# Performance work log

Hardware: AMD Instinct MI355X
Metric: run time of the kernel (lower is better)

The kernel has to match this reference:

```python
import jax, jax.numpy as jnp
import numpy as np

W = 5      # window size
H = 4      # num heads (num_channels)
EPS = 1e-6

def rmsnorm(x, w):
    return x * w * jax.lax.rsqrt(jnp.mean(x * x, axis=-1, keepdims=True) + EPS)

def dwconv3d(x, k):
    # x: [B,D0,D1,D2,C], k: [3,3,3,1,C] depthwise 3x3x3 conv, SAME padding
    return jax.lax.conv_general_dilated(
        x, k, (1, 1, 1), 'SAME',
        dimension_numbers=('NDHWC', 'DHWIO', 'NDHWC'),
        feature_group_count=x.shape[-1])

def _part(t):
    # [B,D0,D1,D2,C] -> [B*nw, W^3, C] non-overlapping 3D windows
    B, D0, D1, D2, C = t.shape
    t = t.reshape(B, D0 // W, W, D1 // W, W, D2 // W, W, C)
    t = t.transpose(0, 1, 3, 5, 2, 4, 6, 7)
    return t.reshape(-1, W ** 3, C)

def _unpart(t, B, D0, D1, D2):
    C = t.shape[-1]
    t = t.reshape(B, D0 // W, D1 // W, D2 // W, W, W, W, C)
    t = t.transpose(0, 1, 4, 2, 5, 3, 6, 7)
    return t.reshape(B, D0, D1, D2, C)

def _pool01(t):
    # mean-pool poolable_dims=(0,1) by factor W -> coarse grid
    B, D0, D1, D2, C = t.shape
    return t.reshape(B, D0 // W, W, D1 // W, W, D2, C).mean(axis=(2, 4))

def _mha(q, k, v):
    # q,k,v: [N, L, C] -> [N, L, C] multi-head attention
    N, L, C = q.shape
    dh = C // H
    q = q.reshape(N, L, H, dh)
    k = k.reshape(N, L, H, dh)
    v = v.reshape(N, L, H, dh)
    s = jnp.einsum('nqhd,nkhd->nhqk', q, k) * (1.0 / np.sqrt(dh))
    p = jax.nn.softmax(s, axis=-1)
    return jnp.einsum('nhqk,nkhd->nqhd', p, v).reshape(N, L, C)

def _hier_attn(x, qkv_w, qkv_b, proj_w, proj_b, dw_pre, dw_post, lr_down, lr_up):
    B, D0, D1, D2, C = x.shape
    # conv_position='both': pre depthwise-conv positional term
    xin = x + dwconv3d(x, dw_pre)
    qkv = xin @ qkv_w + qkv_b                     # [B,D0,D1,D2,3C]
    q, k, v = jnp.split(qkv, 3, axis=-1)
    # fine scale: windowed local attention in W^3 blocks
    fine = _unpart(_mha(_part(q), _part(k), _part(v)), B, D0, D1, D2)
    # coarse scale: pool dims (0,1) by W, global attention over coarse tokens
    qc, kc, vc = _pool01(q), _pool01(k), _pool01(v)
    Nc = qc.shape[1] * qc.shape[2] * qc.shape[3]
    oc = _mha(qc.reshape(B, Nc, C), kc.reshape(B, Nc, C), vc.reshape(B, Nc, C))
    oc = oc.reshape(B, D0 // W, D1 // W, D2, C)
    oc = jnp.repeat(jnp.repeat(oc, W, axis=1), W, axis=2)   # upsample to full grid
    # lowrank hierarchical merge of coarse branch into fine branch
    merged = fine + (oc @ lr_down) @ lr_up
    out = merged @ proj_w + proj_b
    out = out + xin                               # attn_residual
    out = out + dwconv3d(out, dw_post)            # post conv position
    return out

def setup_inputs() -> dict:
    key = jax.random.key(0)
    ks = jax.random.split(key, 8)
    B, D0, D1, D2, C = 4, 40, 40, 20, 256
    rank = C // 4
    s = 0.02
    return {
        'x': jax.random.normal(ks[0], (B, D0, D1, D2, C), jnp.float32),
        'norm1_w': jnp.ones((C,), jnp.float32),
        'attn_norm_w': jnp.ones((C,), jnp.float32),
        'qkv_w': jax.random.normal(ks[1], (C, 3 * C), jnp.float32) * s,
        'qkv_b': jnp.zeros((3 * C,), jnp.float32),
        'proj_w': jax.random.normal(ks[2], (C, C), jnp.float32) * s,
        'proj_b': jnp.zeros((C,), jnp.float32),
        'dw_pre': jax.random.normal(ks[3], (3, 3, 3, 1, C), jnp.float32) * s,
        'dw_post': jax.random.normal(ks[4], (3, 3, 3, 1, C), jnp.float32) * s,
        'lr_down': jax.random.normal(ks[5], (C, rank), jnp.float32) * s,
        'lr_up': jax.random.normal(ks[6], (rank, C), jnp.float32) * s,
    }

def reference(x, norm1_w, attn_norm_w, qkv_w, qkv_b, proj_w, proj_b,
              dw_pre, dw_post, lr_down, lr_up) -> jnp.ndarray:
    # x = x + attn_norm(hier_attn(norm1(x)))   (dropout inactive in eval)
    a = _hier_attn(rmsnorm(x, norm1_w), qkv_w, qkv_b, proj_w, proj_b,
                   dw_pre, dw_post, lr_down, lr_up)
    return x + rmsnorm(a, attn_norm_w)
```

## Files before the change

### kernel.cpp

```cpp
#include <hip/hip_runtime.h>

#define D0c 40
#define D1c 40
#define D2c 20
#define NVOX 128000

typedef __attribute__((ext_vector_type(4))) float f4;
typedef __attribute__((ext_vector_type(8))) __bf16 bf8;
typedef __attribute__((ext_vector_type(8))) unsigned short u8s;

static __device__ __forceinline__ unsigned short f2bf(float f) {
  union { float f; unsigned int u; } v; v.f = f;
  unsigned int r = v.u + 0x7fffu + ((v.u >> 16) & 1u);
  return (unsigned short)(r >> 16);
}
static __device__ __forceinline__ float bf2f(unsigned short h) {
  union { unsigned int u; float f; } v; v.u = ((unsigned int)h) << 16;
  return v.f;
}

#define MFMA16(a, b, c) __builtin_amdgcn_mfma_f32_16x16x32_bf16((a), (b), (c), 0, 0, 0)

static __device__ __forceinline__ void gload16(const void* g, void* l) {
  __builtin_amdgcn_global_load_lds((const __attribute__((address_space(1))) unsigned int*)g,
                                   (__attribute__((address_space(3))) unsigned int*)l, 16, 0, 0);
}

__global__ __launch_bounds__(256) void k_prepw(const float* __restrict__ qkv_w,
                                               const float* __restrict__ proj_w,
                                               unsigned short* __restrict__ wq,
                                               unsigned short* __restrict__ wp) {
  int id = blockIdx.x * 256 + threadIdx.x;
  if (id < 768 * 256) {
    int kk = id & 31, row = (id >> 5) & 127, kc = (id >> 12) & 7, nt = id >> 15;
    int s = kk >> 3, kj = kk & 7;
    int g = s ^ ((row >> 1) & 3);
    int k = kc * 32 + g * 8 + kj;
    int n = nt * 128 + row;
    wq[id] = f2bf(qkv_w[k * 768 + n]);
  } else {
    int j = id - 768 * 256;
    int kk = j & 31, row = (j >> 5) & 127, kc = (j >> 12) & 7, nt = j >> 15;
    int s = kk >> 3, kj = kk & 7;
    int g = s ^ ((row >> 1) & 3);
    int k = kc * 32 + g * 8 + kj;
    int n = nt * 128 + row;
    wp[j] = f2bf(proj_w[k * 256 + n]);
  }
}

__global__ __launch_bounds__(256) void k_rms1(const float* __restrict__ x,
                                              const float* __restrict__ w,
                                              unsigned short* __restrict__ xn) {
  int wv = threadIdx.x >> 6, ln = threadIdx.x & 63;
  int n = blockIdx.x * 4 + wv;
  f4 v = ((const f4*)(x + (size_t)n * 256))[ln];
  float ss = v.x * v.x + v.y * v.y + v.z * v.z + v.w * v.w;
#pragma unroll
  for (int m = 32; m >= 1; m >>= 1) ss += __shfl_xor(ss, m);
  float rs = rsqrtf(ss * (1.f / 256.f) + 1e-6f);
  f4 wv4 = ((const f4*)w)[ln];
  ushort4 o;
  o.x = f2bf(v.x * wv4.x * rs); o.y = f2bf(v.y * wv4.y * rs);
  o.z = f2bf(v.z * wv4.z * rs); o.w = f2bf(v.w * wv4.w * rs);
  ((ushort4*)(xn + (size_t)n * 256))[ln] = o;
}

__global__ __launch_bounds__(256) void k_convpre(const unsigned short* __restrict__ xn,
                                                 const float* __restrict__ dw,
                                                 unsigned short* __restrict__ xin) {
  __shared__ float wl[6912];
  for (int i = threadIdx.x; i < 6912; i += 256) wl[i] = dw[i];
  __syncthreads();
  int wv = threadIdx.x >> 6, ln = threadIdx.x & 63;
  int col = blockIdx.x * 4 + wv;
  int z1 = col % D1c; int t = col / D1c; int z0 = t % D0c; int b = t / D0c;
  int c0 = ln * 4;

  const unsigned short* base[9];
  bool val[9];
#pragma unroll
  for (int c = 0; c < 9; c++) {
    int dy = c / 3 - 1, dx = c % 3 - 1;
    int y0 = z0 + dy, y1 = z1 + dx;
    val[c] = ((unsigned)y0 < (unsigned)D0c) && ((unsigned)y1 < (unsigned)D1c);
    int yy0 = val[c] ? y0 : z0, yy1 = val[c] ? y1 : z1;
    base[c] = xn + ((size_t)((b * D0c + yy0) * D1c + yy1) * D2c) * 256 + c0;
  }
  f4 a0 = {0.f,0.f,0.f,0.f}, a1 = {0.f,0.f,0.f,0.f}, a2 = {0.f,0.f,0.f,0.f};
  ushort4 nxt[9];
#pragma unroll
  for (int c = 0; c < 9; c++) {
    ushort4 ld = {0, 0, 0, 0};
    if (val[c]) ld = *(const ushort4*)(base[c]);
    nxt[c] = ld;
  }
  unsigned short* op = xin + ((size_t)col * D2c) * 256 + c0;

  for (int z = 0; z < 20; z++) {
    f4 cf[9];
#pragma unroll
    for (int c = 0; c < 9; c++) {
      cf[c].x = bf2f(nxt[c].x); cf[c].y = bf2f(nxt[c].y);
      cf[c].z = bf2f(nxt[c].z); cf[c].w = bf2f(nxt[c].w);
    }
    int zn = (z < 19) ? (z + 1) : 19;
#pragma unroll
    for (int c = 0; c < 9; c++) {
      ushort4 ld = {0, 0, 0, 0};
      if (val[c]) ld = *(const ushort4*)(base[c] + (size_t)zn * 256);
      nxt[c] = ld;
    }
#pragma unroll
    for (int c = 0; c < 9; c++) {
      const f4 w0 = *(const f4*)&wl[(c * 3 + 0) * 256 + c0];
      const f4 w1 = *(const f4*)&wl[(c * 3 + 1) * 256 + c0];
      const f4 w2 = *(const f4*)&wl[(c * 3 + 2) * 256 + c0];
      a0.x += w2.x * cf[c].x; a0.y += w2.y * cf[c].y; a0.z += w2.z * cf[c].z; a0.w += w2.w * cf[c].w;
      a1.x += w1.x * cf[c].x; a1.y += w1.y * cf[c].y; a1.z += w1.z * cf[c].z; a1.w += w1.w * cf[c].w;
      a2.x += w0.x * cf[c].x; a2.y += w0.y * cf[c].y; a2.z += w0.z * cf[c].z; a2.w += w0.w * cf[c].w;
    }
    a1.x += cf[4].x; a1.y += cf[4].y; a1.z += cf[4].z; a1.w += cf[4].w;
    if (z >= 1) {
      ushort4 o;
      o.x = f2bf(a0.x); o.y = f2bf(a0.y); o.z = f2bf(a0.z); o.w = f2bf(a0.w);
      *(ushort4*)op = o;
      op += 256;
    }
    a0 = a1; a1 = a2; a2 = (f4){0.f,0.f,0.f,0.f};
  }
  {
    ushort4 o;
    o.x = f2bf(a0.x); o.y = f2bf(a0.y); o.z = f2bf(a0.z); o.w = f2bf(a0.w);
    *(ushort4*)op = o;
  }
}

__global__ __launch_bounds__(256) void k_gemm_qkv(const unsigned short* __restrict__ a_bf,
                                                  const unsigned short* __restrict__ wq2,
                                                  const float* __restrict__ bias,
                                                  unsigned short* __restrict__ out) {
  __shared__ unsigned short As[16384];
  __shared__ unsigned short Bs[8192];
  int m0 = blockIdx.x * 64;
  int tid = threadIdx.x;
  int w = tid >> 6, l = tid & 63;
  int wr = w >> 1, wc = w & 1;
  int lrow = l & 15, lg = l >> 4;

  {
    const char* Ab = (const char*)(a_bf + (size_t)m0 * 256);
    int row = tid >> 2, s = tid & 3;
    int g = s ^ ((row >> 1) & 3);
    const char* src0 = Ab + row * 512 + g * 16;
    char* dst0 = ((char*)As) + w * 1024 + l * 16;
#pragma unroll
    for (int kc = 0; kc < 8; kc++)
      gload16(src0 + kc * 64, dst0 + kc * 4096);
  }
  {
    const char* gB = (const char*)wq2;
    char* lB = (char*)Bs;
    gload16(gB + tid * 16, lB + w * 1024 + l * 16);
    gload16(gB + 4096 + tid * 16, lB + 4096 + w * 1024 + l * 16);
  }

  int buf = 0;
  f4 acc[2][4];
  for (int nt = 0; nt < 6; nt++) {
    float bvv[4];
#pragma unroll
    for (int j = 0; j < 4; j++) bvv[j] = bias[nt * 128 + wc * 64 + j * 16 + lrow];
#pragma unroll
    for (int i = 0; i < 2; i++)
#pragma unroll
      for (int j = 0; j < 4; j++) acc[i][j] = {0.f, 0.f, 0.f, 0.f};

    for (int kc = 0; kc < 8; kc++) {
      int t = nt * 8 + kc;
      if (t + 1 < 48) {
        const char* gB = (const char*)wq2 + (size_t)(t + 1) * 8192;
        char* lB = ((char*)Bs) + (buf ^ 1) * 8192;
        gload16(gB + tid * 16, lB + w * 1024 + l * 16);
        gload16(gB + 4096 + tid * 16, lB + 4096 + w * 1024 + l * 16);
        asm volatile("s_waitcnt vmcnt(2)\n\ts_barrier" ::: "memory");
      } else {
        asm volatile("s_waitcnt vmcnt(0)\n\ts_barrier" ::: "memory");
      }
      bf8 af[2], bf_[4];
#pragma unroll
      for (int i = 0; i < 2; i++) {
        int row = wr * 32 + i * 16 + lrow;
        af[i] = *(const bf8*)&As[kc * 2048 + row * 32 + ((lg ^ ((row >> 1) & 3)) * 8)];
      }
#pragma unroll
      for (int j = 0; j < 4; j++) {
        int rowb = wc * 64 + j * 16 + lrow;
        bf_[j] = *(const bf8*)&Bs[buf * 4096 + rowb * 32 + ((lg ^ ((rowb >> 1) & 3)) * 8)];
      }
#pragma unroll
      for (int i = 0; i < 2; i++)
#pragma unroll
        for (int j = 0; j < 4; j++) acc[i][j] = MFMA16(af[i], bf_[j], acc[i][j]);
      asm volatile("s_barrier" ::: "memory");
      buf ^= 1;
    }

    unsigned short* Cs = &Bs[(buf ^ 1) * 4096];
    int crow = tid >> 3, cseg = tid & 7;
#pragma unroll
    for (int h = 0; h < 2; h++) {
      if (wr == h) {
#pragma unroll
        for (int i = 0; i < 2; i++)
#pragma unroll
          for (int j = 0; j < 4; j++)
#pragma unroll
            for (int r = 0; r < 4; r++)
              Cs[(i * 16 + lg * 4 + r) * 128 + wc * 64 + j * 16 + lrow] =
                  f2bf(acc[i][j][r] + bvv[j]);
      }
      asm volatile("s_waitcnt lgkmcnt(0)\n\ts_barrier" ::: "memory");
      {
        u8s v0 = *(const u8s*)&Cs[crow * 128 + cseg * 16];
        u8s v1 = *(const u8s*)&Cs[crow * 128 + cseg * 16 + 8];
        unsigned short* orow = out + (size_t)(m0 + h * 32 + crow) * 768 + nt * 128 + cseg * 16;
        *(u8s*)orow = v0;
        *(u8s*)(orow + 8) = v1;
      }
      asm volatile("s_waitcnt lgkmcnt(0)\n\ts_barrier" ::: "memory");
    }
  }
}

__global__ __launch_bounds__(256) void k_fineattn(const unsigned short* __restrict__ qkv,
                                                  unsigned short* __restrict__ fine) {
  __shared__ unsigned short sm[27136];
  unsigned short* Qs = sm;
  unsigned short* Ks = sm + 9216;
  unsigned short* Vt = sm + 18432;
  unsigned short* Ps = sm;
  int h = blockIdx.x & 3, wid = blockIdx.x >> 2;
  int w2 = wid & 3, w1 = (wid >> 2) & 7, w0 = (wid >> 5) & 7, b = wid >> 8;
  int tid = threadIdx.x;
  int tok = tid >> 1, half = tid & 1;
  if (tok < 125) {
    int i0 = tok / 25, rr = tok % 25, i1 = rr / 5, i2 = rr % 5;
    int n = ((b * D0c + w0 * 5 + i0) * D1c + w1 * 5 + i1) * D2c + w2 * 5 + i2;
    const u8s* qp = (const u8s*)(qkv + (size_t)n * 768 + h * 64 + half * 32);
    const u8s* kp = (const u8s*)(qkv + (size_t)n * 768 + 256 + h * 64 + half * 32);
    const unsigned short* vp = qkv + (size_t)n * 768 + 512 + h * 64 + half * 32;
#pragma unroll
    for (int e = 0; e < 4; e++) {
      *(u8s*)&Qs[tok * 72 + half * 32 + e * 8] = qp[e];
      *(u8s*)&Ks[tok * 72 + half * 32 + e * 8] = kp[e];
    }
#pragma unroll
    for (int d = 0; d < 32; d++) Vt[(half * 32 + d) * 136 + tok] = vp[d];
  } else {
    u8s z = {0, 0, 0, 0, 0, 0, 0, 0};
#pragma unroll
    for (int e = 0; e < 4; e++) {
      *(u8s*)&Qs[tok * 72 + half * 32 + e * 8] = z;
      *(u8s*)&Ks[tok * 72 + half * 32 + e * 8] = z;
    }
#pragma unroll
    for (int d = 0; d < 32; d++) Vt[(half * 32 + d) * 136 + tok] = 0;
  }
  __syncthreads();
  int wv = tid >> 6, ln = tid & 63, lrow = ln & 15, lg = ln >> 4;
  f4 s[2][8];
#pragma unroll
  for (int mi = 0; mi < 2; mi++)
#pragma unroll
    for (int ni = 0; ni < 8; ni++) s[mi][ni] = {0.f, 0.f, 0.f, 0.f};
  bf8 aq[2][2];
#pragma unroll
  for (int ks = 0; ks < 2; ks++)
#pragma unroll
    for (int mi = 0; mi < 2; mi++)
      aq[mi][ks] = *(const bf8*)&Qs[(wv * 32 + mi * 16 + lrow) * 72 + ks * 32 + lg * 8];
#pragma unroll
  for (int ni = 0; ni < 8; ni++) {
#pragma unroll
    for (int ks = 0; ks < 2; ks++) {
      bf8 bk = *(const bf8*)&Ks[(ni * 16 + lrow) * 72 + ks * 32 + lg * 8];
      s[0][ni] = MFMA16(aq[0][ks], bk, s[0][ni]);
      s[1][ni] = MFMA16(aq[1][ks], bk, s[1][ni]);
    }
  }
#pragma unroll
  for (int mi = 0; mi < 2; mi++) {
#pragma unroll
    for (int j = 0; j < 4; j++) {
      float mx = -3e38f;
#pragma unroll
      for (int ni = 0; ni < 8; ni++) {
        int col = ni * 16 + lrow;
        float v = (col < 125) ? s[mi][ni][j] * 0.125f : -3e38f;
        s[mi][ni][j] = v;
        mx = fmaxf(mx, v);
      }
#pragma unroll
      for (int m = 8; m >= 1; m >>= 1) mx = fmaxf(mx, __shfl_xor(mx, m));
      float sum = 0.f;
#pragma unroll
      for (int ni = 0; ni < 8; ni++) {
        float p = __expf(s[mi][ni][j] - mx);
        s[mi][ni][j] = p;
        sum += p;
      }
#pragma unroll
      for (int m = 8; m >= 1; m >>= 1) sum += __shfl_xor(sum, m);
      float inv = 1.f / sum;
#pragma unroll
      for (int ni = 0; ni < 8; ni++) s[mi][ni][j] *= inv;
    }
  }
  __syncthreads();
#pragma unroll
  for (int mi = 0; mi < 2; mi++)
#pragma unroll
    for (int ni = 0; ni < 8; ni++)
#pragma unroll
      for (int j = 0; j < 4; j++)
        Ps[(wv * 32 + mi * 16 + lg * 4 + j) * 136 + ni * 16 + lrow] = f2bf(s[mi][ni][j]);
  __syncthreads();
  f4 o[2][4];
#pragma unroll
  for (int mi = 0; mi < 2; mi++)
#pragma unroll
    for (int ni = 0; ni < 4; ni++) o[mi][ni] = {0.f, 0.f, 0.f, 0.f};
#pragma unroll
  for (int ks = 0; ks < 4; ks++) {
    bf8 ap0 = *(const bf8*)&Ps[(wv * 32 + 0 + lrow) * 136 + ks * 32 + lg * 8];
    bf8 ap1 = *(const bf8*)&Ps[(wv * 32 + 16 + lrow) * 136 + ks * 32 + lg * 8];
#pragma unroll
    for (int ni = 0; ni < 4; ni++) {
      bf8 bv = *(const bf8*)&Vt[(ni * 16 + lrow) * 136 + ks * 32 + lg * 8];
      o[0][ni] = MFMA16(ap0, bv, o[0][ni]);
      o[1][ni] = MFMA16(ap1, bv, o[1][ni]);
    }
  }
#pragma unroll
  for (int mi = 0; mi < 2; mi++) {
    int rt0 = wv * 32 + mi * 16 + lg * 4;
#pragma unroll
    for (int r = 0; r < 4; r++) {
      int tk = rt0 + r;
      if (tk >= 125) continue;
      int i0 = tk / 25, rr = tk % 25, i1 = rr / 5, i2 = rr % 5;
      int n = ((b * D0c + w0 * 5 + i0) * D1c + w1 * 5 + i1) * D2c + w2 * 5 + i2;
#pragma unroll
      for (int ni = 0; ni < 4; ni++)
        fine[(size_t)n * 256 + h * 64 + ni * 16 + lrow] = f2bf(o[mi][ni][r]);
    }
  }
}

__global__ __launch_bounds__(256) void k_pool(const unsigned short* __restrict__ qkv,
                                              unsigned short* __restrict__ qc,
                                              unsigned short* __restrict__ kc,
                                              unsigned short* __restrict__ vct) {
  int ct = blockIdx.x;
  int z2 = ct % 20; int t = ct / 20; int c1 = t & 7; int c0 = (t >> 3) & 7; int b = t >> 6;
  int tid = threadIdx.x;
  float a0 = 0.f, a1 = 0.f, a2 = 0.f;
  for (int i0 = 0; i0 < 5; i0++)
    for (int i1 = 0; i1 < 5; i1++) {
      int n = ((b * D0c + c0 * 5 + i0) * D1c + c1 * 5 + i1) * D2c + z2;
      const unsigned short* row = qkv + (size_t)n * 768;
      a0 += bf2f(row[tid]);
      a1 += bf2f(row[tid + 256]);
      a2 += bf2f(row[tid + 512]);
    }
  const float sc = 1.f / 25.f;
  qc[(size_t)ct * 256 + tid] = f2bf(a0 * sc);
  kc[(size_t)ct * 256 + tid] = f2bf(a1 * sc);
  int h = tid >> 6, d = tid & 63;
  int tk = ct - b * 1280;
  vct[(((size_t)b * 4 + h) * 64 + d) * 1288 + tk] = f2bf(a2 * sc);
}

__global__ __launch_bounds__(256) void k_coarse(const unsigned short* __restrict__ qc,
                                                const unsigned short* __restrict__ kc,
                                                const unsigned short* __restrict__ vct,
                                                float* __restrict__ oc) {
  __shared__ unsigned short Qs[9216];
  __shared__ unsigned short KP[9216];
  __shared__ unsigned short Vts[4608];
  int qt = blockIdx.x;
  int b = blockIdx.y >> 2, h = blockIdx.y & 3;
  int tid = threadIdx.x, wv = tid >> 6, ln = tid & 63, lrow = ln & 15, lg = ln >> 4;
  {
    int tk = tid >> 1, half = tid & 1;
    const u8s* qp = (const u8s*)(qc + (size_t)(b * 1280 + qt * 128 + tk) * 256 + h * 64 + half * 32);
#pragma unroll
    for (int e = 0; e < 4; e++) *(u8s*)&Qs[tk * 72 + half * 32 + e * 8] = qp[e];
  }
  float mrun[2][4], srun[2][4];
  f4 o[2][4];
#pragma unroll
  for (int mi = 0; mi < 2; mi++)
#pragma unroll
    for (int j = 0; j < 4; j++) { mrun[mi][j] = -3e38f; srun[mi][j] = 0.f; }
#pragma unroll
  for (int mi = 0; mi < 2; mi++)
#pragma unroll
    for (int ni = 0; ni < 4; ni++) o[mi][ni] = {0.f, 0.f, 0.f, 0.f};

  int ktok = tid >> 2, kq = (tid & 3) * 16;
  int vd = tid >> 2, vtc = (tid & 3) * 16;

  for (int kt = 0; kt < 20; kt++) {
    {
      const u8s* kp = (const u8s*)(kc + (size_t)(b * 1280 + kt * 64 + ktok) * 256 + h * 64 + kq);
      *(u8s*)&KP[ktok * 72 + kq] = kp[0];
      *(u8s*)&KP[ktok * 72 + kq + 8] = kp[1];
      const u8s* vp = (const u8s*)(vct + (((size_t)b * 4 + h) * 64 + vd) * 1288 + kt * 64 + vtc);
      *(u8s*)&Vts[vd * 72 + vtc] = vp[0];
      *(u8s*)&Vts[vd * 72 + vtc + 8] = vp[1];
    }
    __syncthreads();
    f4 s[2][4];
#pragma unroll
    for (int mi = 0; mi < 2; mi++)
#pragma unroll
      for (int ni = 0; ni < 4; ni++) s[mi][ni] = {0.f, 0.f, 0.f, 0.f};
    bf8 aq[2][2];
#pragma unroll
    for (int ks = 0; ks < 2; ks++)
#pragma unroll
      for (int mi = 0; mi < 2; mi++)
        aq[mi][ks] = *(const bf8*)&Qs[(wv * 32 + mi * 16 + lrow) * 72 + ks * 32 + lg * 8];
#pragma unroll
    for (int ni = 0; ni < 4; ni++) {
#pragma unroll
      for (int ks = 0; ks < 2; ks++) {
        bf8 bk = *(const bf8*)&KP[(ni * 16 + lrow) * 72 + ks * 32 + lg * 8];
        s[0][ni] = MFMA16(aq[0][ks], bk, s[0][ni]);
        s[1][ni] = MFMA16(aq[1][ks], bk, s[1][ni]);
      }
    }
#pragma unroll
    for (int mi = 0; mi < 2; mi++) {
#pragma unroll
      for (int j = 0; j < 4; j++) {
        float mx = -3e38f;
#pragma unroll
        for (int ni = 0; ni < 4; ni++) {
          float v = s[mi][ni][j] * 0.125f;
          s[mi][ni][j] = v;
          mx = fmaxf(mx, v);
        }
#pragma unroll
        for (int m = 8; m >= 1; m >>= 1) mx = fmaxf(mx, __shfl_xor(mx, m));
        float nm = fmaxf(mrun[mi][j], mx);
        float alpha = __expf(mrun[mi][j] - nm);
        mrun[mi][j] = nm;
        float sum = 0.f;
#pragma unroll
        for (int ni = 0; ni < 4; ni++) {
          float p = __expf(s[mi][ni][j] - nm);
          s[mi][ni][j] = p;
          sum += p;
        }
#pragma unroll
        for (int m = 8; m >= 1; m >>= 1) sum += __shfl_xor(sum, m);
        srun[mi][j] = srun[mi][j] * alpha + sum;
#pragma unroll
        for (int ni = 0; ni < 4; ni++) o[mi][ni][j] *= alpha;
      }
    }
    __syncthreads();
#pragma unroll
    for (int mi = 0; mi < 2; mi++)
#pragma unroll
      for (int ni = 0; ni < 4; ni++)
#pragma unroll
        for (int j = 0; j < 4; j++)
          KP[(wv * 32 + mi * 16 + lg * 4 + j) * 72 + ni * 16 + lrow] = f2bf(s[mi][ni][j]);
    __syncthreads();
#pragma unroll
    for (int ks = 0; ks < 2; ks++) {
      bf8 ap0 = *(const bf8*)&KP[(wv * 32 + 0 + lrow) * 72 + ks * 32 + lg * 8];
      bf8 ap1 = *(const bf8*)&KP[(wv * 32 + 16 + lrow) * 72 + ks * 32 + lg * 8];
#pragma unroll
      for (int ni = 0; ni < 4; ni++) {
        bf8 bv = *(const bf8*)&Vts[(ni * 16 + lrow) * 72 + ks * 32 + lg * 8];
        o[0][ni] = MFMA16(ap0, bv, o[0][ni]);
        o[1][ni] = MFMA16(ap1, bv, o[1][ni]);
      }
    }
    __syncthreads();
  }
#pragma unroll
  for (int mi = 0; mi < 2; mi++)
#pragma unroll
    for (int j = 0; j < 4; j++) {
      float inv = 1.f / srun[mi][j];
      int row = qt * 128 + wv * 32 + mi * 16 + lg * 4 + j;
      float* orow = oc + ((size_t)(b * 1280 + row)) * 256 + h * 64;
#pragma unroll
      for (int ni = 0; ni < 4; ni++) orow[ni * 16 + lrow] = o[mi][ni][j] * inv;
    }
}

__global__ __launch_bounds__(256) void k_lowrank(const float* __restrict__ oc,
                                                 const float* __restrict__ lrd,
                                                 const float* __restrict__ lru,
                                                 float* __restrict__ oclr) {
  __shared__ float tmp[16 * 64];
  int t0 = blockIdx.x * 16;
  int tid = threadIdx.x;
  int i = tid >> 4, r4 = (tid & 15) * 4;
  f4 a = {0.f, 0.f, 0.f, 0.f};
  const float* orow = oc + (size_t)(t0 + i) * 256;
  for (int k = 0; k < 256; k++) {
    float ov = orow[k];
    const f4 w = *(const f4*)&lrd[k * 64 + r4];
    a.x += ov * w.x; a.y += ov * w.y; a.z += ov * w.z; a.w += ov * w.w;
  }
  *(f4*)&tmp[i * 64 + r4] = a;
  __syncthreads();
  int c16 = (tid & 15) * 16;
  f4 acc0 = {0.f,0.f,0.f,0.f}, acc1 = {0.f,0.f,0.f,0.f}, acc2 = {0.f,0.f,0.f,0.f}, acc3 = {0.f,0.f,0.f,0.f};
  for (int r = 0; r < 64; r++) {
    float tv = tmp[i * 64 + r];
    const f4* wr = (const f4*)&lru[r * 256 + c16];
    f4 w0 = wr[0], w1 = wr[1], w2 = wr[2], w3 = wr[3];
    acc0.x += tv * w0.x; acc0.y += tv * w0.y; acc0.z += tv * w0.z; acc0.w += tv * w0.w;
    acc1.x += tv * w1.x; acc1.y += tv * w1.y; acc1.z += tv * w1.z; acc1.w += tv * w1.w;
    acc2.x += tv * w2.x; acc2.y += tv * w2.y; acc2.z += tv * w2.z; acc2.w += tv * w2.w;
    acc3.x += tv * w3.x; acc3.y += tv * w3.y; acc3.z += tv * w3.z; acc3.w += tv * w3.w;
  }
  float* outr = oclr + (size_t)(t0 + i) * 256 + c16;
  *(f4*)&outr[0] = acc0; *(f4*)&outr[4] = acc1; *(f4*)&outr[8] = acc2; *(f4*)&outr[12] = acc3;
}

__global__ __launch_bounds__(256) void k_gemm_proj(const unsigned short* __restrict__ fine,
                                                   const float* __restrict__ oclr,
                                                   const unsigned short* __restrict__ wp2,
                                                   const float* __restrict__ bias,
                                                   const unsigned short* __restrict__ xin,
                                                   unsigned short* __restrict__ out1) {
  __shared__ unsigned short As[16384];
  __shared__ unsigned short Bs[8192];
  int m0 = blockIdx.x * 64;
  int tid = threadIdx.x;
  int w = tid >> 6, l = tid & 63;
  int wr = w >> 1, wc = w & 1;
  int lrow = l & 15, lg = l >> 4;

  {
    const char* gB = (const char*)wp2;
    char* lB = (char*)Bs;
    gload16(gB + tid * 16, lB + w * 1024 + l * 16);
    gload16(gB + 4096 + tid * 16, lB + 4096 + w * 1024 + l * 16);
  }
  {
    int row = tid >> 2, s = tid & 3;
    int g = s ^ ((row >> 1) & 3);
    int nrow = m0 + row;
    int z2 = nrow % D2c; int tt = nrow / D2c; int z1 = tt % D1c; tt /= D1c;
    int z0 = tt % D0c; int bb = tt / D0c;
    int ct = ((bb * 8 + z0 / 5) * 8 + z1 / 5) * 20 + z2;
    const unsigned short* fp = fine + (size_t)nrow * 256 + g * 8;
    const float* cp = oclr + (size_t)ct * 256 + g * 8;
#pragma unroll
    for (int kc = 0; kc < 8; kc++) {
      u8s fv = *(const u8s*)(fp + kc * 32);
      f4 cv0 = *(const f4*)(cp + kc * 32);
      f4 cv1 = *(const f4*)(cp + kc * 32 + 4);
      u8s t0;
      t0[0] = f2bf(bf2f(fv[0]) + cv0.x); t0[1] = f2bf(bf2f(fv[1]) + cv0.y);
      t0[2] = f2bf(bf2f(fv[2]) + cv0.z); t0[3] = f2bf(bf2f(fv[3]) + cv0.w);
      t0[4] = f2bf(bf2f(fv[4]) + cv1.x); t0[5] = f2bf(bf2f(fv[5]) + cv1.y);
      t0[6] = f2bf(bf2f(fv[6]) + cv1.z); t0[7] = f2bf(bf2f(fv[7]) + cv1.w);
      *(u8s*)&As[kc * 2048 + row * 32 + s * 8] = t0;
    }
  }
  asm volatile("s_waitcnt lgkmcnt(0)\n\ts_barrier" ::: "memory");

  int buf = 0;
  f4 acc[2][4];
  for (int nt = 0; nt < 2; nt++) {
    float bvv[4];
#pragma unroll
    for (int j = 0; j < 4; j++) bvv[j] = bias[nt * 128 + wc * 64 + j * 16 + lrow];
#pragma unroll
    for (int i = 0; i < 2; i++)
#pragma unroll
      for (int j = 0; j < 4; j++) acc[i][j] = {0.f, 0.f, 0.f, 0.f};

    for (int kc = 0; kc < 8; kc++) {
      int t = nt * 8 + kc;
      if (t + 1 < 16) {
        const char* gB = (const char*)wp2 + (size_t)(t + 1) * 8192;
        char* lB = ((char*)Bs) + (buf ^ 1) * 8192;
        gload16(gB + tid * 16, lB + w * 1024 + l * 16);
        gload16(gB + 4096 + tid * 16, lB + 4096 + w * 1024 + l * 16);
        asm volatile("s_waitcnt vmcnt(2)\n\ts_barrier" ::: "memory");
      } else {
        asm volatile("s_waitcnt vmcnt(0)\n\ts_barrier" ::: "memory");
      }
      bf8 af[2], bf_[4];
#pragma unroll
      for (int i = 0; i < 2; i++) {
        int row = wr * 32 + i * 16 + lrow;
        af[i] = *(const bf8*)&As[kc * 2048 + row * 32 + ((lg ^ ((row >> 1) & 3)) * 8)];
      }
#pragma unroll
      for (int j = 0; j < 4; j++) {
        int rowb = wc * 64 + j * 16 + lrow;
        bf_[j] = *(const bf8*)&Bs[buf * 4096 + rowb * 32 + ((lg ^ ((rowb >> 1) & 3)) * 8)];
      }
#pragma unroll
      for (int i = 0; i < 2; i++)
#pragma unroll
        for (int j = 0; j < 4; j++) acc[i][j] = MFMA16(af[i], bf_[j], acc[i][j]);
      asm volatile("s_barrier" ::: "memory");
      buf ^= 1;
    }

    unsigned short* Cs = &Bs[(buf ^ 1) * 4096];
    int crow = tid >> 3, cseg = tid & 7;
#pragma unroll
    for (int h = 0; h < 2; h++) {
      if (wr == h) {
#pragma unroll
        for (int i = 0; i < 2; i++)
#pragma unroll
          for (int j = 0; j < 4; j++)
#pragma unroll
            for (int r = 0; r < 4; r++)
              Cs[(i * 16 + lg * 4 + r) * 128 + wc * 64 + j * 16 + lrow] =
                  f2bf(acc[i][j][r] + bvv[j]);
      }
      asm volatile("s_waitcnt lgkmcnt(0)\n\ts_barrier" ::: "memory");
      {
        u8s v0 = *(const u8s*)&Cs[crow * 128 + cseg * 16];
        u8s v1 = *(const u8s*)&Cs[crow * 128 + cseg * 16 + 8];
        const unsigned short* xrow = xin + (size_t)(m0 + h * 32 + crow) * 256 + nt * 128 + cseg * 16;
        u8s x0 = *(const u8s*)xrow;
        u8s x1 = *(const u8s*)(xrow + 8);
        u8s o0, o1;
#pragma unroll
        for (int e = 0; e < 8; e++) {
          o0[e] = f2bf(bf2f(v0[e]) + bf2f(x0[e]));
          o1[e] = f2bf(bf2f(v1[e]) + bf2f(x1[e]));
        }
        unsigned short* orow = out1 + (size_t)(m0 + h * 32 + crow) * 256 + nt * 128 + cseg * 16;
        *(u8s*)orow = o0;
        *(u8s*)(orow + 8) = o1;
      }
      asm volatile("s_waitcnt lgkmcnt(0)\n\ts_barrier" ::: "memory");
    }
  }
}

__global__ __launch_bounds__(256) void k_convpost(const unsigned short* __restrict__ o1,
                                                  const float* __restrict__ dw,
                                                  const float* __restrict__ x,
                                                  const float* __restrict__ anw,
                                                  float* __restrict__ outp) {
  __shared__ float wl[6912];
  for (int i = threadIdx.x; i < 6912; i += 256) wl[i] = dw[i];
  __syncthreads();
  int wv = threadIdx.x >> 6, ln = threadIdx.x & 63;
  int col = blockIdx.x * 4 + wv;
  int z1 = col % D1c; int t = col / D1c; int z0 = t % D0c; int b = t / D0c;
  int c0 = ln * 4;

  const unsigned short* base[9];
  bool val[9];
#pragma unroll
  for (int c = 0; c < 9; c++) {
    int dy = c / 3 - 1, dx = c % 3 - 1;
    int y0 = z0 + dy, y1 = z1 + dx;
    val[c] = ((unsigned)y0 < (unsigned)D0c) && ((unsigned)y1 < (unsigned)D1c);
    int yy0 = val[c] ? y0 : z0, yy1 = val[c] ? y1 : z1;
    base[c] = o1 + ((size_t)((b * D0c + yy0) * D1c + yy1) * D2c) * 256 + c0;
  }
  f4 a0 = {0.f,0.f,0.f,0.f}, a1 = {0.f,0.f,0.f,0.f}, a2 = {0.f,0.f,0.f,0.f};
  ushort4 nxt[9];
#pragma unroll
  for (int c = 0; c < 9; c++) {
    ushort4 ld = {0, 0, 0, 0};
    if (val[c]) ld = *(const ushort4*)(base[c]);
    nxt[c] = ld;
  }
  const f4 wv4 = *(const f4*)(anw + c0);
  const float* xp = x + ((size_t)col * D2c) * 256 + c0;
  float* op = outp + ((size_t)col * D2c) * 256 + c0;

  for (int z = 0; z < 20; z++) {
    f4 cf[9];
#pragma unroll
    for (int c = 0; c < 9; c++) {
      cf[c].x = bf2f(nxt[c].x); cf[c].y = bf2f(nxt[c].y);
      cf[c].z = bf2f(nxt[c].z); cf[c].w = bf2f(nxt[c].w);
    }
    int zn = (z < 19) ? (z + 1) : 19;
#pragma unroll
    for (int c = 0; c < 9; c++) {
      ushort4 ld = {0, 0, 0, 0};
      if (val[c]) ld = *(const ushort4*)(base[c] + (size_t)zn * 256);
      nxt[c] = ld;
    }
#pragma unroll
    for (int c = 0; c < 9; c++) {
      const f4 w0 = *(const f4*)&wl[(c * 3 + 0) * 256 + c0];
      const f4 w1 = *(const f4*)&wl[(c * 3 + 1) * 256 + c0];
      const f4 w2 = *(const f4*)&wl[(c * 3 + 2) * 256 + c0];
      a0.x += w2.x * cf[c].x; a0.y += w2.y * cf[c].y; a0.z += w2.z * cf[c].z; a0.w += w2.w * cf[c].w;
      a1.x += w1.x * cf[c].x; a1.y += w1.y * cf[c].y; a1.z += w1.z * cf[c].z; a1.w += w1.w * cf[c].w;
      a2.x += w0.x * cf[c].x; a2.y += w0.y * cf[c].y; a2.z += w0.z * cf[c].z; a2.w += w0.w * cf[c].w;
    }
    a1.x += cf[4].x; a1.y += cf[4].y; a1.z += cf[4].z; a1.w += cf[4].w;
    if (z >= 1) {
      float ss = a0.x * a0.x + a0.y * a0.y + a0.z * a0.z + a0.w * a0.w;
#pragma unroll
      for (int m = 32; m >= 1; m >>= 1) ss += __shfl_xor(ss, m);
      float rs = rsqrtf(ss * (1.f / 256.f) + 1e-6f);
      f4 xv = *(const f4*)xp;
      f4 res;
      res.x = xv.x + a0.x * wv4.x * rs;
      res.y = xv.y + a0.y * wv4.y * rs;
      res.z = xv.z + a0.z * wv4.z * rs;
      res.w = xv.w + a0.w * wv4.w * rs;
      *(f4*)op = res;
      xp += 256; op += 256;
    }
    a0 = a1; a1 = a2; a2 = (f4){0.f,0.f,0.f,0.f};
  }
  {
    float ss = a0.x * a0.x + a0.y * a0.y + a0.z * a0.z + a0.w * a0.w;
#pragma unroll
    for (int m = 32; m >= 1; m >>= 1) ss += __shfl_xor(ss, m);
    float rs = rsqrtf(ss * (1.f / 256.f) + 1e-6f);
    f4 xv = *(const f4*)xp;
    f4 res;
    res.x = xv.x + a0.x * wv4.x * rs;
    res.y = xv.y + a0.y * wv4.y * rs;
    res.z = xv.z + a0.z * wv4.z * rs;
    res.w = xv.w + a0.w * wv4.w * rs;
    *(f4*)op = res;
  }
}

extern "C" void kernel_launch(void* const* d_in, const int* in_sizes, int n_in,
                              void* d_out, int out_size, void* d_ws, size_t ws_size,
                              hipStream_t stream) {
  const float* x          = (const float*)d_in[0];
  const float* norm1_w    = (const float*)d_in[1];
  const float* attn_norm_w= (const float*)d_in[2];
  const float* qkv_w      = (const float*)d_in[3];
  const float* qkv_b      = (const float*)d_in[4];
  const float* proj_w     = (const float*)d_in[5];
  const float* proj_b     = (const float*)d_in[6];
  const float* dw_pre     = (const float*)d_in[7];
  const float* dw_post    = (const float*)d_in[8];
  const float* lr_down    = (const float*)d_in[9];
  const float* lr_up      = (const float*)d_in[10];
  float* outp = (float*)d_out;

  unsigned char* w = (unsigned char*)d_ws;
  size_t off = 0;
  unsigned short* xn   = (unsigned short*)(w + off); off += 65536000ULL;
  unsigned short* xin  = (unsigned short*)(w + off); off += 65536000ULL;
  unsigned short* qkv  = (unsigned short*)(w + off); off += 196608000ULL;
  unsigned short* out1 = (unsigned short*)(w + off); off += 65536000ULL;
  unsigned short* qc   = (unsigned short*)(w + off); off += 2621440ULL;
  unsigned short* kc   = (unsigned short*)(w + off); off += 2621440ULL;
  unsigned short* vct  = (unsigned short*)(w + off); off += 2637824ULL;
  float* oc            = (float*)(w + off);          off += 5242880ULL;
  float* oclr          = (float*)(w + off);          off += 5242880ULL;
  unsigned short* wq   = (unsigned short*)(w + off); off += 393216ULL;
  unsigned short* wp   = (unsigned short*)(w + off); off += 131072ULL;
  unsigned short* fine = xn;

  k_prepw<<<1024, 256, 0, stream>>>(qkv_w, proj_w, wq, wp);
  k_rms1<<<32000, 256, 0, stream>>>(x, norm1_w, xn);
  k_convpre<<<1600, 256, 0, stream>>>(xn, dw_pre, xin);
  k_gemm_qkv<<<2000, 256, 0, stream>>>(xin, wq, qkv_b, qkv);
  k_fineattn<<<4096, 256, 0, stream>>>(qkv, fine);
  k_pool<<<5120, 256, 0, stream>>>(qkv, qc, kc, vct);
  k_coarse<<<dim3(10, 16), 256, 0, stream>>>(qc, kc, vct, oc);
  k_lowrank<<<320, 256, 0, stream>>>(oc, lr_down, lr_up, oclr);
  k_gemm_proj<<<2000, 256, 0, stream>>>(fine, oclr, wp, proj_b, xin, out1);
  k_convpost<<<1600, 256, 0, stream>>>(out1, dw_post, x, attn_norm_w, outp);
}
```

Baseline: 668.5 us.

## Remap depthwise convs to one channel per thread and vectorize pooling loads

Both depthwise 3D conv kernels now give each block a single spatial column, with one thread per channel. The 27 weights are held in registers instead of staging a 27x256 table into shared memory, and there are four times as many blocks. The post conv's RMS reduction therefore crosses waves, using shared memory and a __syncthreads on every z step. The pooling kernel uses 96 threads, each loading 8 contiguous bf16 values with a vector load, which replaces three scalar loads per thread. The trade-off is narrower 2-byte global loads and stores in the convs plus extra barriers in the post conv, in exchange for more parallelism and no shared-memory weight staging.

```diff
diff --git a/kernel.cpp b/kernel.cpp
--- a/kernel.cpp
+++ b/kernel.cpp
@@ -69,13 +69,13 @@
 __global__ __launch_bounds__(256) void k_convpre(const unsigned short* __restrict__ xn,
                                                  const float* __restrict__ dw,
                                                  unsigned short* __restrict__ xin) {
-  __shared__ float wl[6912];
-  for (int i = threadIdx.x; i < 6912; i += 256) wl[i] = dw[i];
-  __syncthreads();
-  int wv = threadIdx.x >> 6, ln = threadIdx.x & 63;
-  int col = blockIdx.x * 4 + wv;
+  int ch = threadIdx.x;
+  int col = blockIdx.x;
   int z1 = col % D1c; int t = col / D1c; int z0 = t % D0c; int b = t / D0c;
-  int c0 = ln * 4;
+
+  float W[27];
+#pragma unroll
+  for (int k = 0; k < 27; k++) W[k] = dw[k * 256 + ch];
 
   const unsigned short* base[9];
   bool val[9];
@@ -85,55 +85,36 @@
     int y0 = z0 + dy, y1 = z1 + dx;
     val[c] = ((unsigned)y0 < (unsigned)D0c) && ((unsigned)y1 < (unsigned)D1c);
     int yy0 = val[c] ? y0 : z0, yy1 = val[c] ? y1 : z1;
-    base[c] = xn + ((size_t)((b * D0c + yy0) * D1c + yy1) * D2c) * 256 + c0;
-  }
-  f4 a0 = {0.f,0.f,0.f,0.f}, a1 = {0.f,0.f,0.f,0.f}, a2 = {0.f,0.f,0.f,0.f};
-  ushort4 nxt[9];
-#pragma unroll
-  for (int c = 0; c < 9; c++) {
-    ushort4 ld = {0, 0, 0, 0};
-    if (val[c]) ld = *(const ushort4*)(base[c]);
-    nxt[c] = ld;
-  }
-  unsigned short* op = xin + ((size_t)col * D2c) * 256 + c0;
+    base[c] = xn + ((size_t)((b * D0c + yy0) * D1c + yy1) * D2c) * 256 + ch;
+  }
+  float a0 = 0.f, a1 = 0.f, a2 = 0.f;
+  unsigned short nxt[9];
+#pragma unroll
+  for (int c = 0; c < 9; c++) nxt[c] = val[c] ? base[c][0] : (unsigned short)0;
+  unsigned short* op = xin + ((size_t)col * D2c) * 256 + ch;
 
   for (int z = 0; z < 20; z++) {
-    f4 cf[9];
+    float cf[9];
+#pragma unroll
+    for (int c = 0; c < 9; c++) cf[c] = bf2f(nxt[c]);
+    int zn = (z < 19) ? (z + 1) : 19;
+#pragma unroll
+    for (int c = 0; c < 9; c++)
+      nxt[c] = val[c] ? base[c][(size_t)zn * 256] : (unsigned short)0;
 #pragma unroll
     for (int c = 0; c < 9; c++) {
-      cf[c].x = bf2f(nxt[c].x); cf[c].y = bf2f(nxt[c].y);
-      cf[c].z = bf2f(nxt[c].z); cf[c].w = bf2f(nxt[c].w);
-    }
-    int zn = (z < 19) ? (z + 1) : 19;
-#pragma unroll
-    for (int c = 0; c < 9; c++) {
-      ushort4 ld = {0, 0, 0, 0};
-      if (val[c]) ld = *(const ushort4*)(base[c] + (size_t)zn * 256);
-      nxt[c] = ld;
-    }
-#pragma unroll
-    for (int c = 0; c < 9; c++) {
-      const f4 w0 = *(const f4*)&wl[(c * 3 + 0) * 256 + c0];
-      const f4 w1 = *(const f4*)&wl[(c * 3 + 1) * 256 + c0];
-      const f4 w2 = *(const f4*)&wl[(c * 3 + 2) * 256 + c0];
-      a0.x += w2.x * cf[c].x; a0.y += w2.y * cf[c].y; a0.z += w2.z * cf[c].z; a0.w += w2.w * cf[c].w;
-      a1.x += w1.x * cf[c].x; a1.y += w1.y * cf[c].y; a1.z += w1.z * cf[c].z; a1.w += w1.w * cf[c].w;
-      a2.x += w0.x * cf[c].x; a2.y += w0.y * cf[c].y; a2.z += w0.z * cf[c].z; a2.w += w0.w * cf[c].w;
-    }
-    a1.x += cf[4].x; a1.y += cf[4].y; a1.z += cf[4].z; a1.w += cf[4].w;
+      a0 += W[c * 3 + 2] * cf[c];
+      a1 += W[c * 3 + 1] * cf[c];
+      a2 += W[c * 3 + 0] * cf[c];
+    }
+    a1 += cf[4];
     if (z >= 1) {
-      ushort4 o;
-      o.x = f2bf(a0.x); o.y = f2bf(a0.y); o.z = f2bf(a0.z); o.w = f2bf(a0.w);
-      *(ushort4*)op = o;
+      *op = f2bf(a0);
       op += 256;
     }
-    a0 = a1; a1 = a2; a2 = (f4){0.f,0.f,0.f,0.f};
-  }
-  {
-    ushort4 o;
-    o.x = f2bf(a0.x); o.y = f2bf(a0.y); o.z = f2bf(a0.z); o.w = f2bf(a0.w);
-    *(ushort4*)op = o;
-  }
+    a0 = a1; a1 = a2; a2 = 0.f;
+  }
+  *op = f2bf(a0);
 }
 
 __global__ __launch_bounds__(256) void k_gemm_qkv(const unsigned short* __restrict__ a_bf,
@@ -358,28 +339,43 @@
   }
 }
 
-__global__ __launch_bounds__(256) void k_pool(const unsigned short* __restrict__ qkv,
+__global__ __launch_bounds__(128) void k_pool(const unsigned short* __restrict__ qkv,
                                               unsigned short* __restrict__ qc,
                                               unsigned short* __restrict__ kc,
                                               unsigned short* __restrict__ vct) {
   int ct = blockIdx.x;
+  int tid = threadIdx.x;
+  if (tid >= 96) return;
   int z2 = ct % 20; int t = ct / 20; int c1 = t & 7; int c0 = (t >> 3) & 7; int b = t >> 6;
-  int tid = threadIdx.x;
-  float a0 = 0.f, a1 = 0.f, a2 = 0.f;
+  int off = tid * 8;
+  f4 s0 = {0.f, 0.f, 0.f, 0.f}, s1 = {0.f, 0.f, 0.f, 0.f};
   for (int i0 = 0; i0 < 5; i0++)
     for (int i1 = 0; i1 < 5; i1++) {
       int n = ((b * D0c + c0 * 5 + i0) * D1c + c1 * 5 + i1) * D2c + z2;
-      const unsigned short* row = qkv + (size_t)n * 768;
-      a0 += bf2f(row[tid]);
-      a1 += bf2f(row[tid + 256]);
-      a2 += bf2f(row[tid + 512]);
+      u8s v = *(const u8s*)(qkv + (size_t)n * 768 + off);
+      s0.x += bf2f(v[0]); s0.y += bf2f(v[1]); s0.z += bf2f(v[2]); s0.w += bf2f(v[3]);
+      s1.x += bf2f(v[4]); s1.y += bf2f(v[5]); s1.z += bf2f(v[6]); s1.w += bf2f(v[7]);
     }
   const float sc = 1.f / 25.f;
-  qc[(size_t)ct * 256 + tid] = f2bf(a0 * sc);
-  kc[(size_t)ct * 256 + tid] = f2bf(a1 * sc);
-  int h = tid >> 6, d = tid & 63;
-  int tk = ct - b * 1280;
-  vct[(((size_t)b * 4 + h) * 64 + d) * 1288 + tk] = f2bf(a2 * sc);
+  s0.x *= sc; s0.y *= sc; s0.z *= sc; s0.w *= sc;
+  s1.x *= sc; s1.y *= sc; s1.z *= sc; s1.w *= sc;
+  if (off < 512) {
+    unsigned short* dst = (off < 256) ? (qc + (size_t)ct * 256 + off)
+                                      : (kc + (size_t)ct * 256 + (off - 256));
+    u8s o;
+    o[0] = f2bf(s0.x); o[1] = f2bf(s0.y); o[2] = f2bf(s0.z); o[3] = f2bf(s0.w);
+    o[4] = f2bf(s1.x); o[5] = f2bf(s1.y); o[6] = f2bf(s1.z); o[7] = f2bf(s1.w);
+    *(u8s*)dst = o;
+  } else {
+    int vch = off - 512;
+    int h = vch >> 6, d0 = vch & 63;
+    int tk = ct - b * 1280;
+    unsigned short* vb = vct + (((size_t)b * 4 + h) * 64 + d0) * 1288 + tk;
+    vb[0 * 1288] = f2bf(s0.x); vb[1 * 1288] = f2bf(s0.y);
+    vb[2 * 1288] = f2bf(s0.z); vb[3 * 1288] = f2bf(s0.w);
+    vb[4 * 1288] = f2bf(s1.x); vb[5 * 1288] = f2bf(s1.y);
+    vb[6 * 1288] = f2bf(s1.z); vb[7 * 1288] = f2bf(s1.w);
+  }
 }
 
 __global__ __launch_bounds__(256) void k_coarse(const unsigned short* __restrict__ qc,
@@ -664,13 +660,15 @@
                                                   const float* __restrict__ x,
                                                   const float* __restrict__ anw,
                                                   float* __restrict__ outp) {
-  __shared__ float wl[6912];
-  for (int i = threadIdx.x; i < 6912; i += 256) wl[i] = dw[i];
-  __syncthreads();
-  int wv = threadIdx.x >> 6, ln = threadIdx.x & 63;
-  int col = blockIdx.x * 4 + wv;
+  __shared__ float red[2][4];
+  int ch = threadIdx.x, wv = ch >> 6, ln = ch & 63;
+  int col = blockIdx.x;
   int z1 = col % D1c; int t = col / D1c; int z0 = t % D0c; int b = t / D0c;
-  int c0 = ln * 4;
+
+  float W[27];
+#pragma unroll
+  for (int k = 0; k < 27; k++) W[k] = dw[k * 256 + ch];
+  float wn = anw[ch];
 
   const unsigned short* base[9];
   bool val[9];
@@ -680,72 +678,53 @@
     int y0 = z0 + dy, y1 = z1 + dx;
     val[c] = ((unsigned)y0 < (unsigned)D0c) && ((unsigned)y1 < (unsigned)D1c);
     int yy0 = val[c] ? y0 : z0, yy1 = val[c] ? y1 : z1;
-    base[c] = o1 + ((size_t)((b * D0c + yy0) * D1c + yy1) * D2c) * 256 + c0;
-  }
-  f4 a0 = {0.f,0.f,0.f,0.f}, a1 = {0.f,0.f,0.f,0.f}, a2 = {0.f,0.f,0.f,0.f};
-  ushort4 nxt[9];
-#pragma unroll
-  for (int c = 0; c < 9; c++) {
-    ushort4 ld = {0, 0, 0, 0};
-    if (val[c]) ld = *(const ushort4*)(base[c]);
-    nxt[c] = ld;
-  }
-  const f4 wv4 = *(const f4*)(anw + c0);
-  const float* xp = x + ((size_t)col * D2c) * 256 + c0;
-  float* op = outp + ((size_t)col * D2c) * 256 + c0;
+    base[c] = o1 + ((size_t)((b * D0c + yy0) * D1c + yy1) * D2c) * 256 + ch;
+  }
+  float a0 = 0.f, a1 = 0.f, a2 = 0.f;
+  unsigned short nxt[9];
+#pragma unroll
+  for (int c = 0; c < 9; c++) nxt[c] = val[c] ? base[c][0] : (unsigned short)0;
+  const float* xp = x + ((size_t)col * D2c) * 256 + ch;
+  float* op = outp + ((size_t)col * D2c) * 256 + ch;
 
   for (int z = 0; z < 20; z++) {
-    f4 cf[9];
+    float cf[9];
+#pragma unroll
+    for (int c = 0; c < 9; c++) cf[c] = bf2f(nxt[c]);
+    int zn = (z < 19) ? (z + 1) : 19;
+#pragma unroll
+    for (int c = 0; c < 9; c++)
+      nxt[c] = val[c] ? base[c][(size_t)zn * 256] : (unsigned short)0;
 #pragma unroll
     for (int c = 0; c < 9; c++) {
-      cf[c].x = bf2f(nxt[c].x); cf[c].y = bf2f(nxt[c].y);
-      cf[c].z = bf2f(nxt[c].z); cf[c].w = bf2f(nxt[c].w);
-    }
-    int zn = (z < 19) ? (z + 1) : 19;
-#pragma unroll
-    for (int c = 0; c < 9; c++) {
-      ushort4 ld = {0, 0, 0, 0};
-      if (val[c]) ld = *(const ushort4*)(base[c] + (size_t)zn * 256);
-      nxt[c] = ld;
-    }
-#pragma unroll
-    for (int c = 0; c < 9; c++) {
-      const f4 w0 = *(const f4*)&wl[(c * 3 + 0) * 256 + c0];
-      const f4 w1 = *(const f4*)&wl[(c * 3 + 1) * 256 + c0];
-      const f4 w2 = *(const f4*)&wl[(c * 3 + 2) * 256 + c0];
-      a0.x += w2.x * cf[c].x; a0.y += w2.y * cf[c].y; a0.z += w2.z * cf[c].z; a0.w += w2.w * cf[c].w;
-      a1.x += w1.x * cf[c].x; a1.y += w1.y * cf[c].y; a1.z += w1.z * cf[c].z; a1.w += w1.w * cf[c].w;
-      a2.x += w0.x * cf[c].x; a2.y += w0.y * cf[c].y; a2.z += w0.z * cf[c].z; a2.w += w0.w * cf[c].w;
-    }
-    a1.x += cf[4].x; a1.y += cf[4].y; a1.z += cf[4].z; a1.w += cf[4].w;
+      a0 += W[c * 3 + 2] * cf[c];
+      a1 += W[c * 3 + 1] * cf[c];
+      a2 += W[c * 3 + 0] * cf[c];
+    }
+    a1 += cf[4];
     if (z >= 1) {
-      float ss = a0.x * a0.x + a0.y * a0.y + a0.z * a0.z + a0.w * a0.w;
+      float ss = a0 * a0;
 #pragma unroll
       for (int m = 32; m >= 1; m >>= 1) ss += __shfl_xor(ss, m);
-      float rs = rsqrtf(ss * (1.f / 256.f) + 1e-6f);
-      f4 xv = *(const f4*)xp;
-      f4 res;
-      res.x = xv.x + a0.x * wv4.x * rs;
-      res.y = xv.y + a0.y * wv4.y * rs;
-      res.z = xv.z + a0.z * wv4.z * rs;
-      res.w = xv.w + a0.w * wv4.w * rs;
-      *(f4*)op = res;
-      xp += 256; op += 256;
-    }
-    a0 = a1; a1 = a2; a2 = (f4){0.f,0.f,0.f,0.f};
+      int par = z & 1;
+      if (ln == 0) red[par][wv] = ss;
+      __syncthreads();
+      float tot = red[par][0] + red[par][1] + red[par][2] + red[par][3];
+      float rs = rsqrtf(tot * (1.f / 256.f) + 1e-6f);
+      *op = *xp + a0 * wn * rs;
+      op += 256; xp += 256;
+    }
+    a0 = a1; a1 = a2; a2 = 0.f;
   }
   {
-    float ss = a0.x * a0.x + a0.y * a0.y + a0.z * a0.z + a0.w * a0.w;
+    float ss = a0 * a0;
 #pragma unroll
     for (int m = 32; m >= 1; m >>= 1) ss += __shfl_xor(ss, m);
-    float rs = rsqrtf(ss * (1.f / 256.f) + 1e-6f);
-    f4 xv = *(const f4*)xp;
-    f4 res;
-    res.x = xv.x + a0.x * wv4.x * rs;
-    res.y = xv.y + a0.y * wv4.y * rs;
-    res.z = xv.z + a0.z * wv4.z * rs;
-    res.w = xv.w + a0.w * wv4.w * rs;
-    *(f4*)op = res;
+    if (ln == 0) red[0][wv] = ss;
+    __syncthreads();
+    float tot = red[0][0] + red[0][1] + red[0][2] + red[0][3];
+    float rs = rsqrtf(tot * (1.f / 256.f) + 1e-6f);
+    *op = *xp + a0 * wn * rs;
   }
 }
 
@@ -782,12 +761,12 @@
 
   k_prepw<<<1024, 256, 0, stream>>>(qkv_w, proj_w, wq, wp);
   k_rms1<<<32000, 256, 0, stream>>>(x, norm1_w, xn);
-  k_convpre<<<1600, 256, 0, stream>>>(xn, dw_pre, xin);
+  k_convpre<<<6400, 256, 0, stream>>>(xn, dw_pre, xin);
   k_gemm_qkv<<<2000, 256, 0, stream>>>(xin, wq, qkv_b, qkv);
   k_fineattn<<<4096, 256, 0, stream>>>(qkv, fine);
-  k_pool<<<5120, 256, 0, stream>>>(qkv, qc, kc, vct);
+  k_pool<<<5120, 128, 0, stream>>>(qkv, qc, kc, vct);
   k_coarse<<<dim3(10, 16), 256, 0, stream>>>(qc, kc, vct, oc);
   k_lowrank<<<320, 256, 0, stream>>>(oc, lr_down, lr_up, oclr);
   k_gemm_proj<<<2000, 256, 0, stream>>>(fine, oclr, wp, proj_b, xin, out1);
-  k_convpost<<<1600, 256, 0, stream>>>(out1, dw_post, x, attn_norm_w, outp);
-}
+  k_convpost<<<6400, 256, 0, stream>>>(out1, dw_post, x, attn_norm_w, outp);
+}
```

Result: slower. 701.8 us (+5.0%).
